# Performance work log

Hardware: AMD Instinct MI355X
Metric: run time of the kernel (lower is better)

## Reference

```python
import jax, jax.numpy as jnp
import numpy as np

D_MODEL = 512
N_HEAD = 8
D_HEAD = D_MODEL // N_HEAD
EPS = 1e-6


def setup_inputs() -> dict:
    key = jax.random.key(0)
    ks = jax.random.split(key, 11)
    b, s, d = 4, 8192, D_MODEL
    scale = 1.0 / np.sqrt(d)
    inp = {
        "q": jax.random.normal(ks[0], (b, s, d), jnp.float32),
        "k": jax.random.normal(ks[1], (b, s, d), jnp.float32),
        "v": jax.random.normal(ks[2], (b, s, d), jnp.float32),
        "Wq": jax.random.normal(ks[3], (d, d), jnp.float32) * scale,
        "bq": jax.random.normal(ks[4], (d,), jnp.float32) * 0.01,
        "Wk": jax.random.normal(ks[5], (d, d), jnp.float32) * scale,
        "bk": jax.random.normal(ks[6], (d,), jnp.float32) * 0.01,
        "Wv": jax.random.normal(ks[7], (d, d), jnp.float32) * scale,
        "bv": jax.random.normal(ks[8], (d,), jnp.float32) * 0.01,
        "Wo": jax.random.normal(ks[9], (d, d), jnp.float32) * scale,
        "bo": jax.random.normal(ks[10], (d,), jnp.float32) * 0.01,
    }
    return inp


def reference(q, k, v, Wq, bq, Wk, bk, Wv, bv, Wo, bo):
    b, s, d = q.shape
    # torch nn.Linear: x @ W.T + b
    feat = lambda x, W, bias: jax.nn.elu(
        (x @ W.T + bias).reshape(b, s, N_HEAD, D_HEAD)) + 1.0
    queries = feat(q, Wq, bq)                      # [b,s,h,dh]
    keys = feat(k, Wk, bk)                         # [b,s,h,dh]
    values = (v @ Wv.T + bv).reshape(b, s, N_HEAD, D_HEAD)
    # full-sequence KV summary state
    k_v = jnp.einsum('bshd,bshm->bhdm', keys, values)   # [b,h,dh,dh]
    z = keys.sum(axis=1, keepdims=True)                 # [b,1,h,dh]
    num = jnp.einsum('bshd,bhdm->bshm', queries, k_v)   # [b,s,h,dh]
    den = jnp.sum(queries * z, axis=-1)                 # [b,s,h] (broadcast over s)
    out = num / (den[..., None] + EPS)
    out = out.reshape(b, s, d)
    return (out @ Wo.T + bo, k_v, z)
```

## Files before the change

kernel.cpp:

```cpp
#include <hip/hip_runtime.h>
#include <hip/hip_bf16.h>
#include <stdint.h>

typedef __bf16 bf16x8 __attribute__((ext_vector_type(8)));
typedef float f32x4 __attribute__((ext_vector_type(4)));

#define S_LEN 8192
#define BATCH 4
#define DMODEL 512
#define NHEAD 8
#define DHEAD 64
#define MROWS (BATCH * S_LEN)
#define OUT0_ELEMS (MROWS * DMODEL)
#define KV_ELEMS (BATCH * NHEAD * DHEAD * DHEAD)
#define Z_ELEMS (BATCH * NHEAD * DHEAD)

__device__ __forceinline__ uint16_t f2bf(float f) {
    uint32_t u = __float_as_uint(f);
    u = (u + 0x7fffu + ((u >> 16) & 1u)) >> 16;
    return (uint16_t)u;
}
__device__ __forceinline__ uint32_t pack2(float a, float b) {
    union { __hip_bfloat162 h; uint32_t u; } cv;
    cv.h = __float22bfloat162_rn(make_float2(a, b));
    return cv.u;
}
__device__ __forceinline__ void gload_lds16(const void* g, void* l) {
    __builtin_amdgcn_global_load_lds(
        (const __attribute__((address_space(1))) void*)g,
        (__attribute__((address_space(3))) void*)l, 16, 0, 0);
}

__global__ void wconv_kernel(const float* __restrict__ w0, const float* __restrict__ w1,
                             const float* __restrict__ w2, const float* __restrict__ w3,
                             uint16_t* __restrict__ dst) {
    const float* src = (blockIdx.y == 0) ? w0 : (blockIdx.y == 1) ? w1
                       : (blockIdx.y == 2) ? w2 : w3;
    uint16_t* d = dst + (size_t)blockIdx.y * (DMODEL * DMODEL);
    int i = (blockIdx.x * 256 + threadIdx.x) * 4;
    float4 v = *(const float4*)(src + i);
    uint2 o;
    o.x = pack2(v.x, v.y);
    o.y = pack2(v.z, v.w);
    *(uint2*)(d + i) = o;
}

template<bool A_F32, bool ELU1, bool OUT_F32, bool OUT_TRANS>
__global__ __launch_bounds__(256, 3)
void gemm_kernel(const void* __restrict__ Ap, const uint16_t* __restrict__ Wb,
                 const float* __restrict__ bias, void* __restrict__ Cp)
{
    __shared__ uint4 smem4[1280];
    uint16_t* sA = (uint16_t*)smem4;
    uint16_t* sB = (uint16_t*)(smem4 + 512);
    const int tid = threadIdx.x;
    const int lane = tid & 63, w = tid >> 6;
    const int quad = lane >> 4, l15 = lane & 15;
    const int m_blk = blockIdx.x * 128, n_blk = blockIdx.y * 128;

    f32x4 acc[4][4];
#pragma unroll
    for (int mi = 0; mi < 4; ++mi)
#pragma unroll
        for (int ni = 0; ni < 4; ++ni) acc[mi][ni] = (f32x4){0.f, 0.f, 0.f, 0.f};

    const int ar = tid >> 1;
    const int ah = tid & 1;
    const int g0 = w * 2;

    const float* arow_base = A_F32 ? ((const float*)Ap + (size_t)(m_blk + ar) * 512 + ah * 16)
                                   : nullptr;
    float4 a0, a1, a2, a3;
    if (A_F32) {
        a0 = *(const float4*)(arow_base);
        a1 = *(const float4*)(arow_base + 4);
        a2 = *(const float4*)(arow_base + 8);
        a3 = *(const float4*)(arow_base + 12);
    }

    for (int kk = 0; kk < 16; ++kk) {
        const int k0 = kk * 32;
        uint4 p0, p1;
        float4 b0, b1, b2, b3;
        if (A_F32) {
            if (kk < 15) {
                const float* arow = arow_base + (kk + 1) * 32;
                b0 = *(const float4*)(arow);
                b1 = *(const float4*)(arow + 4);
                b2 = *(const float4*)(arow + 8);
                b3 = *(const float4*)(arow + 12);
            }
            p0 = make_uint4(pack2(a0.x, a0.y), pack2(a0.z, a0.w),
                            pack2(a1.x, a1.y), pack2(a1.z, a1.w));
            p1 = make_uint4(pack2(a2.x, a2.y), pack2(a2.z, a2.w),
                            pack2(a3.x, a3.y), pack2(a3.z, a3.w));
        }
        __syncthreads();
        gload_lds16(Wb + (size_t)(n_blk + g0 * 16 + l15) * 512 + k0 + quad * 8,
                    sB + g0 * 512);
        gload_lds16(Wb + (size_t)(n_blk + (g0 + 1) * 16 + l15) * 512 + k0 + quad * 8,
                    sB + (g0 + 1) * 512);
        if (A_F32) {
            uint16_t* base = sA + (((ar >> 4) * 4 + ah * 2) * 16 + (ar & 15)) * 8;
            *(uint4*)base = p0;
            *(uint4*)(base + 128) = p1;
            if (kk < 15) { a0 = b0; a1 = b1; a2 = b2; a3 = b3; }
        } else {
            const uint16_t* Ab = (const uint16_t*)Ap;
            gload_lds16(Ab + (size_t)(m_blk + g0 * 16 + l15) * 512 + k0 + quad * 8,
                        sA + g0 * 512);
            gload_lds16(Ab + (size_t)(m_blk + (g0 + 1) * 16 + l15) * 512 + k0 + quad * 8,
                        sA + (g0 + 1) * 512);
        }
        __syncthreads();
        bf16x8 afr[4], bfr[4];
#pragma unroll
        for (int mi = 0; mi < 4; ++mi)
            afr[mi] = *(const bf16x8*)(sA + (((w & 1) * 4 + mi) * 64 + lane) * 8);
#pragma unroll
        for (int ni = 0; ni < 4; ++ni)
            bfr[ni] = *(const bf16x8*)(sB + (((w >> 1) * 4 + ni) * 64 + lane) * 8);
#pragma unroll
        for (int mi = 0; mi < 4; ++mi)
#pragma unroll
            for (int ni = 0; ni < 4; ++ni)
                acc[mi][ni] = __builtin_amdgcn_mfma_f32_16x16x32_bf16(
                    afr[mi], bfr[ni], acc[mi][ni], 0, 0, 0);
    }
    __syncthreads();

    const int mw = (w & 1) * 64, nw = (w >> 1) * 64;
    float bias4[4];
#pragma unroll
    for (int ni = 0; ni < 4; ++ni) bias4[ni] = bias[n_blk + nw + ni * 16 + l15];

    if (OUT_TRANS) {
        uint16_t* t = (uint16_t*)smem4 + w * 2560;
        uint16_t* C = (uint16_t*)Cp;
        const int bb = m_blk >> 13;
        const int s_base = (m_blk & 8191) + mw;
#pragma unroll
        for (int p = 0; p < 2; ++p) {
#pragma unroll
            for (int mi2 = 0; mi2 < 2; ++mi2) {
                const int mi = p * 2 + mi2;
#pragma unroll
                for (int ni = 0; ni < 4; ++ni)
#pragma unroll
                    for (int r = 0; r < 4; ++r) {
                        float val = acc[mi][ni][r] + bias4[ni];
                        if (ELU1) val = (val > 0.f) ? (val + 1.f) : __expf(val);
                        t[(ni * 16 + l15) * 40 + mi2 * 16 + quad * 4 + r] = f2bf(val);
                    }
            }
#pragma unroll
            for (int it = 0; it < 4; ++it) {
                const int idx = it * 64 + lane;
                const int col = idx >> 2, sg = idx & 3;
                uint4 vv = *(const uint4*)(t + col * 40 + sg * 8);
                *(uint4*)(C + ((size_t)(bb * 512) + n_blk + nw + col) * 8192
                            + s_base + p * 32 + sg * 8) = vv;
            }
        }
    } else if (OUT_F32) {
        float* t = (float*)(smem4 + w * 256);
        float* C = (float*)Cp;
#pragma unroll
        for (int mi = 0; mi < 4; ++mi) {
#pragma unroll
            for (int ni = 0; ni < 4; ++ni)
#pragma unroll
                for (int r = 0; r < 4; ++r) {
                    float val = acc[mi][ni][r] + bias4[ni];
                    if (ELU1) val = (val > 0.f) ? (val + 1.f) : __expf(val);
                    t[(quad * 4 + r) * 64 + ni * 16 + l15] = val;
                }
#pragma unroll
            for (int c = 0; c < 4; ++c) {
                const int idx = c * 64 + lane;
                const int row = idx >> 4, colc = (idx & 15) * 4;
                float4 vv = *(const float4*)(t + row * 64 + colc);
                *(float4*)(C + (size_t)(m_blk + mw + mi * 16 + row) * 512
                             + n_blk + nw + colc) = vv;
            }
        }
    } else {
        uint16_t* t = (uint16_t*)(smem4 + w * 128);
        uint16_t* C = (uint16_t*)Cp;
#pragma unroll
        for (int mi = 0; mi < 4; ++mi) {
#pragma unroll
            for (int ni = 0; ni < 4; ++ni)
#pragma unroll
                for (int r = 0; r < 4; ++r) {
                    float val = acc[mi][ni][r] + bias4[ni];
                    if (ELU1) val = (val > 0.f) ? (val + 1.f) : __expf(val);
                    t[(quad * 4 + r) * 64 + ni * 16 + l15] = f2bf(val);
                }
#pragma unroll
            for (int c = 0; c < 2; ++c) {
                const int idx = c * 64 + lane;
                const int row = idx >> 3, colc = (idx & 7) * 8;
                uint4 vv = *(const uint4*)(t + row * 64 + colc);
                *(uint4*)(C + (size_t)(m_blk + mw + mi * 16 + row) * 512
                            + n_blk + nw + colc) = vv;
            }
        }
    }
}

__global__ __launch_bounds__(256)
void kv_kernel(const uint16_t* __restrict__ KT, const uint16_t* __restrict__ VT,
               float* __restrict__ kvz)
{
    __shared__ uint16_t sA[4096];
    __shared__ uint16_t sB[4096];
    const int tid = threadIdx.x;
    const int lane = tid & 63, w = tid >> 6;
    const int quad = lane >> 4, l15 = lane & 15;
    const int bh = blockIdx.y, b = bh >> 3, h = bh & 7;
    const int dh2 = w & 1, mh2 = w >> 1;
    const int S0 = blockIdx.x * 512;

    const uint16_t* Arow = KT + ((size_t)(b * 512 + h * 64 + w * 16 + l15)) * 8192 + S0;
    const uint16_t* Brow = VT + ((size_t)(b * 512 + h * 64 + w * 16 + l15)) * 8192 + S0;

    f32x4 acc[2][2], accz[2];
#pragma unroll
    for (int mi = 0; mi < 2; ++mi) {
        accz[mi] = (f32x4){0.f, 0.f, 0.f, 0.f};
#pragma unroll
        for (int ni = 0; ni < 2; ++ni) acc[mi][ni] = (f32x4){0.f, 0.f, 0.f, 0.f};
    }
    bf16x8 ones;
#pragma unroll
    for (int j = 0; j < 8; ++j) ones[j] = (__bf16)1.0f;

    for (int it = 0; it < 8; ++it) {
        const int soff = it * 64;
        __syncthreads();
#pragma unroll
        for (int c = 0; c < 2; ++c) {
            gload_lds16(Arow + soff + (quad + 4 * c) * 8, sA + (w * 2 + c) * 512);
            gload_lds16(Brow + soff + (quad + 4 * c) * 8, sB + (w * 2 + c) * 512);
        }
        __syncthreads();
#pragma unroll
        for (int kk = 0; kk < 2; ++kk) {
            bf16x8 afr[2], bfr[2];
#pragma unroll
            for (int mi = 0; mi < 2; ++mi)
                afr[mi] = *(const bf16x8*)(sA + (((dh2 * 2 + mi) * 2 + kk) * 64 + lane) * 8);
#pragma unroll
            for (int ni = 0; ni < 2; ++ni)
                bfr[ni] = *(const bf16x8*)(sB + (((mh2 * 2 + ni) * 2 + kk) * 64 + lane) * 8);
#pragma unroll
            for (int mi = 0; mi < 2; ++mi)
#pragma unroll
                for (int ni = 0; ni < 2; ++ni)
                    acc[mi][ni] = __builtin_amdgcn_mfma_f32_16x16x32_bf16(
                        afr[mi], bfr[ni], acc[mi][ni], 0, 0, 0);
            if (mh2 == 0) {
#pragma unroll
                for (int mi = 0; mi < 2; ++mi)
                    accz[mi] = __builtin_amdgcn_mfma_f32_16x16x32_bf16(
                        afr[mi], ones, accz[mi], 0, 0, 0);
            }
        }
    }
    float* kvp = kvz + (size_t)bh * 4096;
#pragma unroll
    for (int mi = 0; mi < 2; ++mi)
#pragma unroll
        for (int ni = 0; ni < 2; ++ni)
#pragma unroll
            for (int r = 0; r < 4; ++r)
                atomicAdd(kvp + (dh2 * 32 + mi * 16 + quad * 4 + r) * 64
                              + mh2 * 32 + ni * 16 + l15, acc[mi][ni][r]);
    if (mh2 == 0 && l15 == 0) {
#pragma unroll
        for (int mi = 0; mi < 2; ++mi)
#pragma unroll
            for (int r = 0; r < 4; ++r)
                atomicAdd(kvz + KV_ELEMS + bh * 64 + dh2 * 32 + mi * 16 + quad * 4 + r,
                          accz[mi][r]);
    }
}

__global__ void kvf_kernel(const float* __restrict__ kvz, uint16_t* __restrict__ KVf) {
    const int bh = blockIdx.x;
    const int tid = threadIdx.x;
    for (int e = tid; e < 5120; e += 256) {
        const int j = e & 7, c = e >> 3;
        const int l15c = c & 15, quadc = (c >> 4) & 3, kkc = (c >> 6) & 1, ng = c >> 7;
        const int n = ng * 16 + l15c;
        const int d = kkc * 32 + quadc * 8 + j;
        float val = (n < 64) ? kvz[(size_t)bh * 4096 + d * 64 + n]
                  : ((n == 64) ? kvz[KV_ELEMS + bh * 64 + d] : 0.f);
        KVf[(size_t)bh * 5120 + e] = f2bf(val);
    }
}

__global__ __launch_bounds__(256, 4)
void attn_kernel(const uint16_t* __restrict__ Qb, const uint16_t* __restrict__ KVf,
                 uint16_t* __restrict__ Yb)
{
    __shared__ uint4 smem4[1152];
    uint16_t* sB = (uint16_t*)smem4;
    uint16_t* sEp = (uint16_t*)(smem4 + 640);
    const int bh = blockIdx.y;
    const int b = bh >> 3, h = bh & 7;
    const int tid = threadIdx.x;
    const int lane = tid & 63, w = tid >> 6, quad = lane >> 4, l15 = lane & 15;

    const uint16_t* src = KVf + (size_t)bh * 5120;
    gload_lds16(src + (size_t)tid * 8,         sB + (w * 64) * 8);
    gload_lds16(src + (size_t)(256 + tid) * 8, sB + ((256 + w * 64)) * 8);
    if (tid < 128)
        gload_lds16(src + (size_t)(512 + tid) * 8, sB + ((512 + w * 64)) * 8);
    __syncthreads();

    f32x4 acc[2][5];
#pragma unroll
    for (int mi = 0; mi < 2; ++mi)
#pragma unroll
        for (int ni = 0; ni < 5; ++ni) acc[mi][ni] = (f32x4){0.f, 0.f, 0.f, 0.f};
    const int row0 = blockIdx.x * 128 + w * 32;
#pragma unroll
    for (int kk = 0; kk < 2; ++kk) {
        bf16x8 afr[2];
#pragma unroll
        for (int mi = 0; mi < 2; ++mi) {
            const size_t ga = (size_t)(b * S_LEN + row0 + mi * 16 + l15) * DMODEL
                              + h * DHEAD + kk * 32 + quad * 8;
            afr[mi] = *(const bf16x8*)(Qb + ga);
        }
#pragma unroll
        for (int ni = 0; ni < 5; ++ni) {
            bf16x8 bfr = *(const bf16x8*)(sB + ((ni * 2 + kk) * 64 + lane) * 8);
            acc[0][ni] = __builtin_amdgcn_mfma_f32_16x16x32_bf16(afr[0], bfr, acc[0][ni], 0, 0, 0);
            acc[1][ni] = __builtin_amdgcn_mfma_f32_16x16x32_bf16(afr[1], bfr, acc[1][ni], 0, 0, 0);
        }
    }
    uint16_t* t = sEp + w * 1024;
#pragma unroll
    for (int mi = 0; mi < 2; ++mi) {
        float rden[4];
#pragma unroll
        for (int r = 0; r < 4; ++r) {
            const float den = __shfl(acc[mi][4][r], lane & 48, 64);
            rden[r] = 1.0f / (den + 1e-6f);
        }
#pragma unroll
        for (int ni = 0; ni < 4; ++ni)
#pragma unroll
            for (int r = 0; r < 4; ++r)
                t[(quad * 4 + r) * 64 + ni * 16 + l15] = f2bf(acc[mi][ni][r] * rden[r]);
#pragma unroll
        for (int c = 0; c < 2; ++c) {
            const int idx = c * 64 + lane;
            const int row = idx >> 3, colc = (idx & 7) * 8;
            uint4 vv = *(const uint4*)(t + row * 64 + colc);
            *(uint4*)(Yb + (size_t)(b * S_LEN + row0 + mi * 16 + row) * 512
                        + h * DHEAD + colc) = vv;
        }
    }
}

extern "C" void kernel_launch(void* const* d_in, const int* in_sizes, int n_in,
                              void* d_out, int out_size, void* d_ws, size_t ws_size,
                              hipStream_t stream)
{
    const float* q  = (const float*)d_in[0];
    const float* k  = (const float*)d_in[1];
    const float* v  = (const float*)d_in[2];
    const float* Wq = (const float*)d_in[3];
    const float* bq = (const float*)d_in[4];
    const float* Wk = (const float*)d_in[5];
    const float* bk = (const float*)d_in[6];
    const float* Wv = (const float*)d_in[7];
    const float* bv = (const float*)d_in[8];
    const float* Wo = (const float*)d_in[9];
    const float* bo = (const float*)d_in[10];

    uint16_t* Qb = (uint16_t*)d_ws;
    uint16_t* KT = Qb + OUT0_ELEMS;
    uint16_t* VT = KT + OUT0_ELEMS;
    uint16_t* Wb = VT + OUT0_ELEMS;
    uint16_t* KVf = VT;
    uint16_t* Yb = KT;

    float* out0 = (float*)d_out;
    float* kvz  = out0 + OUT0_ELEMS;

    hipMemsetAsync(kvz, 0, (KV_ELEMS + Z_ELEMS) * sizeof(float), stream);
    wconv_kernel<<<dim3(256, 4), 256, 0, stream>>>(Wq, Wk, Wv, Wo, Wb);
    gemm_kernel<true, true,  false, false><<<dim3(256, 4), 256, 0, stream>>>(q, Wb,              bq, Qb);
    gemm_kernel<true, true,  false, true ><<<dim3(256, 4), 256, 0, stream>>>(k, Wb + 262144,     bk, KT);
    gemm_kernel<true, false, false, true ><<<dim3(256, 4), 256, 0, stream>>>(v, Wb + 2 * 262144, bv, VT);
    kv_kernel<<<dim3(16, 32), 256, 0, stream>>>(KT, VT, kvz);
    kvf_kernel<<<dim3(32), 256, 0, stream>>>(kvz, KVf);
    attn_kernel<<<dim3(64, 32), 256, 0, stream>>>(Qb, KVf, Yb);
    gemm_kernel<false, false, true, false><<<dim3(256, 4), 256, 0, stream>>>(Yb, Wb + 3 * 262144, bo, out0);
}
```

Baseline: 416.2 us.

## Load A fragments directly to registers and stage full weight K-slab in LDS

The GEMM kernel stops staging the activation tile in shared memory. Each wave loads its A fragments straight from global memory into registers with one-step prefetch, and the whole 128x512 weight slab is staged in LDS in two halves, so the k-loop needs two barriers instead of thirty-two. The KV reduction kernel likewise drops LDS and reads K/V fragments directly into registers with prefetch, removing its per-iteration barriers. In exchange, LDS use grows to 64KB per block (occupancy hint lowered to 2), and each activation element is now fetched from global memory twice, once by each of the two waves sharing those rows.

```diff
diff --git a/kernel.cpp b/kernel.cpp
--- a/kernel.cpp
+++ b/kernel.cpp
@@ -46,17 +46,17 @@
 }
 
 template<bool A_F32, bool ELU1, bool OUT_F32, bool OUT_TRANS>
-__global__ __launch_bounds__(256, 3)
+__global__ __launch_bounds__(256, 2)
 void gemm_kernel(const void* __restrict__ Ap, const uint16_t* __restrict__ Wb,
                  const float* __restrict__ bias, void* __restrict__ Cp)
 {
-    __shared__ uint4 smem4[1280];
-    uint16_t* sA = (uint16_t*)smem4;
-    uint16_t* sB = (uint16_t*)(smem4 + 512);
+    __shared__ uint4 smem4[4096];
+    uint16_t* sB = (uint16_t*)smem4;
     const int tid = threadIdx.x;
     const int lane = tid & 63, w = tid >> 6;
     const int quad = lane >> 4, l15 = lane & 15;
     const int m_blk = blockIdx.x * 128, n_blk = blockIdx.y * 128;
+    const int mw = (w & 1) * 64, nw = (w >> 1) * 64;
 
     f32x4 acc[4][4];
 #pragma unroll
@@ -64,72 +64,85 @@
 #pragma unroll
         for (int ni = 0; ni < 4; ++ni) acc[mi][ni] = (f32x4){0.f, 0.f, 0.f, 0.f};
 
-    const int ar = tid >> 1;
-    const int ah = tid & 1;
-    const int g0 = w * 2;
-
-    const float* arow_base = A_F32 ? ((const float*)Ap + (size_t)(m_blk + ar) * 512 + ah * 16)
-                                   : nullptr;
-    float4 a0, a1, a2, a3;
-    if (A_F32) {
-        a0 = *(const float4*)(arow_base);
-        a1 = *(const float4*)(arow_base + 4);
-        a2 = *(const float4*)(arow_base + 8);
-        a3 = *(const float4*)(arow_base + 12);
-    }
-
-    for (int kk = 0; kk < 16; ++kk) {
-        const int k0 = kk * 32;
-        uint4 p0, p1;
-        float4 b0, b1, b2, b3;
+    const float* a32[4];
+    const uint16_t* a16[4];
+#pragma unroll
+    for (int mi = 0; mi < 4; ++mi) {
+        const size_t row = (size_t)(m_blk + mw + mi * 16 + l15);
+        if (A_F32) a32[mi] = (const float*)Ap + row * 512 + quad * 8;
+        else       a16[mi] = (const uint16_t*)Ap + row * 512 + quad * 8;
+    }
+
+    float4 ac[4][2];
+    uint4  ac16[4];
+#pragma unroll
+    for (int mi = 0; mi < 4; ++mi) {
         if (A_F32) {
-            if (kk < 15) {
-                const float* arow = arow_base + (kk + 1) * 32;
-                b0 = *(const float4*)(arow);
-                b1 = *(const float4*)(arow + 4);
-                b2 = *(const float4*)(arow + 8);
-                b3 = *(const float4*)(arow + 12);
-            }
-            p0 = make_uint4(pack2(a0.x, a0.y), pack2(a0.z, a0.w),
-                            pack2(a1.x, a1.y), pack2(a1.z, a1.w));
-            p1 = make_uint4(pack2(a2.x, a2.y), pack2(a2.z, a2.w),
-                            pack2(a3.x, a3.y), pack2(a3.z, a3.w));
+            ac[mi][0] = *(const float4*)(a32[mi]);
+            ac[mi][1] = *(const float4*)(a32[mi] + 4);
+        } else {
+            ac16[mi] = *(const uint4*)(a16[mi]);
+        }
+    }
+
+#pragma unroll
+    for (int h = 0; h < 2; ++h) {
+        if (h) __syncthreads();
+#pragma unroll
+        for (int t = 0; t < 16; ++t) {
+            const int f = w * 16 + t;
+            const int nl = f >> 3, kkl = f & 7;
+            gload_lds16(Wb + (size_t)(n_blk + nl * 16 + l15) * 512 + h * 256 + kkl * 32 + quad * 8,
+                        sB + f * 512);
         }
         __syncthreads();
-        gload_lds16(Wb + (size_t)(n_blk + g0 * 16 + l15) * 512 + k0 + quad * 8,
-                    sB + g0 * 512);
-        gload_lds16(Wb + (size_t)(n_blk + (g0 + 1) * 16 + l15) * 512 + k0 + quad * 8,
-                    sB + (g0 + 1) * 512);
-        if (A_F32) {
-            uint16_t* base = sA + (((ar >> 4) * 4 + ah * 2) * 16 + (ar & 15)) * 8;
-            *(uint4*)base = p0;
-            *(uint4*)(base + 128) = p1;
-            if (kk < 15) { a0 = b0; a1 = b1; a2 = b2; a3 = b3; }
-        } else {
-            const uint16_t* Ab = (const uint16_t*)Ap;
-            gload_lds16(Ab + (size_t)(m_blk + g0 * 16 + l15) * 512 + k0 + quad * 8,
-                        sA + g0 * 512);
-            gload_lds16(Ab + (size_t)(m_blk + (g0 + 1) * 16 + l15) * 512 + k0 + quad * 8,
-                        sA + (g0 + 1) * 512);
-        }
-        __syncthreads();
-        bf16x8 afr[4], bfr[4];
-#pragma unroll
-        for (int mi = 0; mi < 4; ++mi)
-            afr[mi] = *(const bf16x8*)(sA + (((w & 1) * 4 + mi) * 64 + lane) * 8);
-#pragma unroll
-        for (int ni = 0; ni < 4; ++ni)
-            bfr[ni] = *(const bf16x8*)(sB + (((w >> 1) * 4 + ni) * 64 + lane) * 8);
-#pragma unroll
-        for (int mi = 0; mi < 4; ++mi)
-#pragma unroll
-            for (int ni = 0; ni < 4; ++ni)
-                acc[mi][ni] = __builtin_amdgcn_mfma_f32_16x16x32_bf16(
-                    afr[mi], bfr[ni], acc[mi][ni], 0, 0, 0);
+#pragma unroll
+        for (int kkl = 0; kkl < 8; ++kkl) {
+            const int kkg = h * 8 + kkl;
+            float4 an[4][2];
+            uint4  an16[4];
+            if (kkg < 15) {
+#pragma unroll
+                for (int mi = 0; mi < 4; ++mi) {
+                    if (A_F32) {
+                        an[mi][0] = *(const float4*)(a32[mi] + (kkg + 1) * 32);
+                        an[mi][1] = *(const float4*)(a32[mi] + (kkg + 1) * 32 + 4);
+                    } else {
+                        an16[mi] = *(const uint4*)(a16[mi] + (kkg + 1) * 32);
+                    }
+                }
+            }
+            bf16x8 afr[4];
+#pragma unroll
+            for (int mi = 0; mi < 4; ++mi) {
+                union { uint4 u; bf16x8 v; } cv;
+                if (A_F32) {
+                    cv.u = make_uint4(pack2(ac[mi][0].x, ac[mi][0].y), pack2(ac[mi][0].z, ac[mi][0].w),
+                                      pack2(ac[mi][1].x, ac[mi][1].y), pack2(ac[mi][1].z, ac[mi][1].w));
+                } else {
+                    cv.u = ac16[mi];
+                }
+                afr[mi] = cv.v;
+            }
+#pragma unroll
+            for (int ni = 0; ni < 4; ++ni) {
+                const bf16x8 bfr = *(const bf16x8*)(sB + ((((w >> 1) * 4 + ni) * 8 + kkl) * 64 + lane) * 8);
+#pragma unroll
+                for (int mi = 0; mi < 4; ++mi)
+                    acc[mi][ni] = __builtin_amdgcn_mfma_f32_16x16x32_bf16(
+                        afr[mi], bfr, acc[mi][ni], 0, 0, 0);
+            }
+            if (kkg < 15) {
+#pragma unroll
+                for (int mi = 0; mi < 4; ++mi) {
+                    if (A_F32) { ac[mi][0] = an[mi][0]; ac[mi][1] = an[mi][1]; }
+                    else       { ac16[mi] = an16[mi]; }
+                }
+            }
+        }
     }
     __syncthreads();
 
-    const int mw = (w & 1) * 64, nw = (w >> 1) * 64;
     float bias4[4];
 #pragma unroll
     for (int ni = 0; ni < 4; ++ni) bias4[ni] = bias[n_blk + nw + ni * 16 + l15];
@@ -209,12 +222,10 @@
     }
 }
 
-__global__ __launch_bounds__(256)
+__global__ __launch_bounds__(256, 4)
 void kv_kernel(const uint16_t* __restrict__ KT, const uint16_t* __restrict__ VT,
                float* __restrict__ kvz)
 {
-    __shared__ uint16_t sA[4096];
-    __shared__ uint16_t sB[4096];
     const int tid = threadIdx.x;
     const int lane = tid & 63, w = tid >> 6;
     const int quad = lane >> 4, l15 = lane & 15;
@@ -222,8 +233,13 @@
     const int dh2 = w & 1, mh2 = w >> 1;
     const int S0 = blockIdx.x * 512;
 
-    const uint16_t* Arow = KT + ((size_t)(b * 512 + h * 64 + w * 16 + l15)) * 8192 + S0;
-    const uint16_t* Brow = VT + ((size_t)(b * 512 + h * 64 + w * 16 + l15)) * 8192 + S0;
+    const uint16_t* Ka[2];
+    const uint16_t* Va[2];
+#pragma unroll
+    for (int i = 0; i < 2; ++i) {
+        Ka[i] = KT + (size_t)(b * 512 + h * 64 + dh2 * 32 + i * 16 + l15) * 8192 + S0 + quad * 8;
+        Va[i] = VT + (size_t)(b * 512 + h * 64 + mh2 * 32 + i * 16 + l15) * 8192 + S0 + quad * 8;
+    }
 
     f32x4 acc[2][2], accz[2];
 #pragma unroll
@@ -236,36 +252,45 @@
 #pragma unroll
     for (int j = 0; j < 8; ++j) ones[j] = (__bf16)1.0f;
 
-    for (int it = 0; it < 8; ++it) {
-        const int soff = it * 64;
-        __syncthreads();
-#pragma unroll
-        for (int c = 0; c < 2; ++c) {
-            gload_lds16(Arow + soff + (quad + 4 * c) * 8, sA + (w * 2 + c) * 512);
-            gload_lds16(Brow + soff + (quad + 4 * c) * 8, sB + (w * 2 + c) * 512);
-        }
-        __syncthreads();
-#pragma unroll
-        for (int kk = 0; kk < 2; ++kk) {
-            bf16x8 afr[2], bfr[2];
+    uint4 ka[2], va[2];
+#pragma unroll
+    for (int i = 0; i < 2; ++i) {
+        ka[i] = *(const uint4*)(Ka[i]);
+        va[i] = *(const uint4*)(Va[i]);
+    }
+
+#pragma unroll
+    for (int it = 0; it < 16; ++it) {
+        uint4 kn[2], vn[2];
+        if (it < 15) {
+#pragma unroll
+            for (int i = 0; i < 2; ++i) {
+                kn[i] = *(const uint4*)(Ka[i] + (it + 1) * 32);
+                vn[i] = *(const uint4*)(Va[i] + (it + 1) * 32);
+            }
+        }
+        bf16x8 afr[2], bfr[2];
+#pragma unroll
+        for (int i = 0; i < 2; ++i) {
+            union { uint4 u; bf16x8 v; } ca, cb;
+            ca.u = ka[i]; afr[i] = ca.v;
+            cb.u = va[i]; bfr[i] = cb.v;
+        }
+#pragma unroll
+        for (int mi = 0; mi < 2; ++mi)
+#pragma unroll
+            for (int ni = 0; ni < 2; ++ni)
+                acc[mi][ni] = __builtin_amdgcn_mfma_f32_16x16x32_bf16(
+                    afr[mi], bfr[ni], acc[mi][ni], 0, 0, 0);
+        if (mh2 == 0) {
 #pragma unroll
             for (int mi = 0; mi < 2; ++mi)
-                afr[mi] = *(const bf16x8*)(sA + (((dh2 * 2 + mi) * 2 + kk) * 64 + lane) * 8);
-#pragma unroll
-            for (int ni = 0; ni < 2; ++ni)
-                bfr[ni] = *(const bf16x8*)(sB + (((mh2 * 2 + ni) * 2 + kk) * 64 + lane) * 8);
-#pragma unroll
-            for (int mi = 0; mi < 2; ++mi)
-#pragma unroll
-                for (int ni = 0; ni < 2; ++ni)
-                    acc[mi][ni] = __builtin_amdgcn_mfma_f32_16x16x32_bf16(
-                        afr[mi], bfr[ni], acc[mi][ni], 0, 0, 0);
-            if (mh2 == 0) {
-#pragma unroll
-                for (int mi = 0; mi < 2; ++mi)
-                    accz[mi] = __builtin_amdgcn_mfma_f32_16x16x32_bf16(
-                        afr[mi], ones, accz[mi], 0, 0, 0);
-            }
+                accz[mi] = __builtin_amdgcn_mfma_f32_16x16x32_bf16(
+                    afr[mi], ones, accz[mi], 0, 0, 0);
+        }
+        if (it < 15) {
+#pragma unroll
+            for (int i = 0; i < 2; ++i) { ka[i] = kn[i]; va[i] = vn[i]; }
         }
     }
     float* kvp = kvz + (size_t)bh * 4096;
```

Result: slower. 501.1 us (+20.4%).

## Double-buffer GEMM LDS tiles and load KV fragments directly into registers

Applied to the files above, without the earlier changes.

The projection GEMM moves from single-buffered LDS staging with two barriers per k-step to a ping-pong pair of A/B LDS buffers. The next tile's loads and packs now overlap the MFMA work on the current tile, with one barrier per half-step. The kv_kernel drops LDS entirely: each wave reads its K/V fragments straight from global memory into registers with one-step prefetch, and it gains a launch-bounds occupancy hint. The costs are more LDS per GEMM block, which can lower occupancy, and redundant global reads in kv_kernel because waves no longer share staged tiles.

```diff
diff --git a/kernel.cpp b/kernel.cpp
--- a/kernel.cpp
+++ b/kernel.cpp
@@ -50,13 +50,16 @@
 void gemm_kernel(const void* __restrict__ Ap, const uint16_t* __restrict__ Wb,
                  const float* __restrict__ bias, void* __restrict__ Cp)
 {
-    __shared__ uint4 smem4[1280];
-    uint16_t* sA = (uint16_t*)smem4;
-    uint16_t* sB = (uint16_t*)(smem4 + 512);
+    __shared__ uint4 smem4[2048];
+    uint16_t* sA0 = (uint16_t*)smem4;
+    uint16_t* sB0 = sA0 + 4096;
+    uint16_t* sA1 = sB0 + 4096;
+    uint16_t* sB1 = sA1 + 4096;
     const int tid = threadIdx.x;
     const int lane = tid & 63, w = tid >> 6;
     const int quad = lane >> 4, l15 = lane & 15;
     const int m_blk = blockIdx.x * 128, n_blk = blockIdx.y * 128;
+    const int g0 = w * 2;
 
     f32x4 acc[4][4];
 #pragma unroll
@@ -66,53 +69,39 @@
 
     const int ar = tid >> 1;
     const int ah = tid & 1;
-    const int g0 = w * 2;
-
     const float* arow_base = A_F32 ? ((const float*)Ap + (size_t)(m_blk + ar) * 512 + ah * 16)
                                    : nullptr;
-    float4 a0, a1, a2, a3;
-    if (A_F32) {
-        a0 = *(const float4*)(arow_base);
-        a1 = *(const float4*)(arow_base + 4);
-        a2 = *(const float4*)(arow_base + 8);
-        a3 = *(const float4*)(arow_base + 12);
-    }
-
-    for (int kk = 0; kk < 16; ++kk) {
-        const int k0 = kk * 32;
-        uint4 p0, p1;
-        float4 b0, b1, b2, b3;
-        if (A_F32) {
-            if (kk < 15) {
-                const float* arow = arow_base + (kk + 1) * 32;
-                b0 = *(const float4*)(arow);
-                b1 = *(const float4*)(arow + 4);
-                b2 = *(const float4*)(arow + 8);
-                b3 = *(const float4*)(arow + 12);
-            }
-            p0 = make_uint4(pack2(a0.x, a0.y), pack2(a0.z, a0.w),
-                            pack2(a1.x, a1.y), pack2(a1.z, a1.w));
-            p1 = make_uint4(pack2(a2.x, a2.y), pack2(a2.z, a2.w),
-                            pack2(a3.x, a3.y), pack2(a3.z, a3.w));
-        }
-        __syncthreads();
+    const uint16_t* Ab = (const uint16_t*)Ap;
+
+    auto loadA = [&](int t, float4* r) {
+        const float* p = arow_base + t * 32;
+        r[0] = *(const float4*)(p);
+        r[1] = *(const float4*)(p + 4);
+        r[2] = *(const float4*)(p + 8);
+        r[3] = *(const float4*)(p + 12);
+    };
+    auto packA = [&](uint16_t* sA, const float4* r) {
+        uint16_t* base = sA + (((ar >> 4) * 4 + ah * 2) * 16 + (ar & 15)) * 8;
+        *(uint4*)base = make_uint4(pack2(r[0].x, r[0].y), pack2(r[0].z, r[0].w),
+                                   pack2(r[1].x, r[1].y), pack2(r[1].z, r[1].w));
+        *(uint4*)(base + 128) = make_uint4(pack2(r[2].x, r[2].y), pack2(r[2].z, r[2].w),
+                                           pack2(r[3].x, r[3].y), pack2(r[3].z, r[3].w));
+    };
+    auto stageB = [&](uint16_t* sB, int t) {
+        const int k0 = t * 32;
         gload_lds16(Wb + (size_t)(n_blk + g0 * 16 + l15) * 512 + k0 + quad * 8,
                     sB + g0 * 512);
         gload_lds16(Wb + (size_t)(n_blk + (g0 + 1) * 16 + l15) * 512 + k0 + quad * 8,
                     sB + (g0 + 1) * 512);
-        if (A_F32) {
-            uint16_t* base = sA + (((ar >> 4) * 4 + ah * 2) * 16 + (ar & 15)) * 8;
-            *(uint4*)base = p0;
-            *(uint4*)(base + 128) = p1;
-            if (kk < 15) { a0 = b0; a1 = b1; a2 = b2; a3 = b3; }
-        } else {
-            const uint16_t* Ab = (const uint16_t*)Ap;
-            gload_lds16(Ab + (size_t)(m_blk + g0 * 16 + l15) * 512 + k0 + quad * 8,
-                        sA + g0 * 512);
-            gload_lds16(Ab + (size_t)(m_blk + (g0 + 1) * 16 + l15) * 512 + k0 + quad * 8,
-                        sA + (g0 + 1) * 512);
-        }
-        __syncthreads();
+    };
+    auto stageA16 = [&](uint16_t* sA, int t) {
+        const int k0 = t * 32;
+        gload_lds16(Ab + (size_t)(m_blk + g0 * 16 + l15) * 512 + k0 + quad * 8,
+                    sA + g0 * 512);
+        gload_lds16(Ab + (size_t)(m_blk + (g0 + 1) * 16 + l15) * 512 + k0 + quad * 8,
+                    sA + (g0 + 1) * 512);
+    };
+    auto compute = [&](const uint16_t* sA, const uint16_t* sB) {
         bf16x8 afr[4], bfr[4];
 #pragma unroll
         for (int mi = 0; mi < 4; ++mi)
@@ -126,8 +115,32 @@
             for (int ni = 0; ni < 4; ++ni)
                 acc[mi][ni] = __builtin_amdgcn_mfma_f32_16x16x32_bf16(
                     afr[mi], bfr[ni], acc[mi][ni], 0, 0, 0);
-    }
+    };
+
+    float4 rX[4], rY[4];
+    if (A_F32) loadA(0, rY);
+    stageB(sB0, 0);
+    if (A_F32) { loadA(1, rX); packA(sA0, rY); }
+    else       stageA16(sA0, 0);
     __syncthreads();
+
+    for (int p = 0; p < 8; ++p) {
+        const int t0 = 2 * p;
+        if (A_F32 && p < 7) loadA(t0 + 2, rY);
+        stageB(sB1, t0 + 1);
+        if (A_F32) packA(sA1, rX);
+        else       stageA16(sA1, t0 + 1);
+        compute(sA0, sB0);
+        __syncthreads();
+        if (p < 7) {
+            if (A_F32) loadA(t0 + 3, rX);
+            stageB(sB0, t0 + 2);
+            if (A_F32) packA(sA0, rY);
+            else       stageA16(sA0, t0 + 2);
+        }
+        compute(sA1, sB1);
+        __syncthreads();
+    }
 
     const int mw = (w & 1) * 64, nw = (w >> 1) * 64;
     float bias4[4];
@@ -209,12 +222,10 @@
     }
 }
 
-__global__ __launch_bounds__(256)
+__global__ __launch_bounds__(256, 4)
 void kv_kernel(const uint16_t* __restrict__ KT, const uint16_t* __restrict__ VT,
                float* __restrict__ kvz)
 {
-    __shared__ uint16_t sA[4096];
-    __shared__ uint16_t sB[4096];
     const int tid = threadIdx.x;
     const int lane = tid & 63, w = tid >> 6;
     const int quad = lane >> 4, l15 = lane & 15;
@@ -222,8 +233,13 @@
     const int dh2 = w & 1, mh2 = w >> 1;
     const int S0 = blockIdx.x * 512;
 
-    const uint16_t* Arow = KT + ((size_t)(b * 512 + h * 64 + w * 16 + l15)) * 8192 + S0;
-    const uint16_t* Brow = VT + ((size_t)(b * 512 + h * 64 + w * 16 + l15)) * 8192 + S0;
+    const uint16_t* Ka[2];
+    const uint16_t* Va[2];
+#pragma unroll
+    for (int i = 0; i < 2; ++i) {
+        Ka[i] = KT + (size_t)(b * 512 + h * 64 + dh2 * 32 + i * 16 + l15) * 8192 + S0 + quad * 8;
+        Va[i] = VT + (size_t)(b * 512 + h * 64 + mh2 * 32 + i * 16 + l15) * 8192 + S0 + quad * 8;
+    }
 
     f32x4 acc[2][2], accz[2];
 #pragma unroll
@@ -236,36 +252,45 @@
 #pragma unroll
     for (int j = 0; j < 8; ++j) ones[j] = (__bf16)1.0f;
 
-    for (int it = 0; it < 8; ++it) {
-        const int soff = it * 64;
-        __syncthreads();
-#pragma unroll
-        for (int c = 0; c < 2; ++c) {
-            gload_lds16(Arow + soff + (quad + 4 * c) * 8, sA + (w * 2 + c) * 512);
-            gload_lds16(Brow + soff + (quad + 4 * c) * 8, sB + (w * 2 + c) * 512);
-        }
-        __syncthreads();
-#pragma unroll
-        for (int kk = 0; kk < 2; ++kk) {
-            bf16x8 afr[2], bfr[2];
+    uint4 ka[2], va[2];
+#pragma unroll
+    for (int i = 0; i < 2; ++i) {
+        ka[i] = *(const uint4*)(Ka[i]);
+        va[i] = *(const uint4*)(Va[i]);
+    }
+
+#pragma unroll
+    for (int it = 0; it < 16; ++it) {
+        uint4 kn[2], vn[2];
+        if (it < 15) {
+#pragma unroll
+            for (int i = 0; i < 2; ++i) {
+                kn[i] = *(const uint4*)(Ka[i] + (it + 1) * 32);
+                vn[i] = *(const uint4*)(Va[i] + (it + 1) * 32);
+            }
+        }
+        bf16x8 afr[2], bfr[2];
+#pragma unroll
+        for (int i = 0; i < 2; ++i) {
+            union { uint4 u; bf16x8 v; } ca, cb;
+            ca.u = ka[i]; afr[i] = ca.v;
+            cb.u = va[i]; bfr[i] = cb.v;
+        }
+#pragma unroll
+        for (int mi = 0; mi < 2; ++mi)
+#pragma unroll
+            for (int ni = 0; ni < 2; ++ni)
+                acc[mi][ni] = __builtin_amdgcn_mfma_f32_16x16x32_bf16(
+                    afr[mi], bfr[ni], acc[mi][ni], 0, 0, 0);
+        if (mh2 == 0) {
 #pragma unroll
             for (int mi = 0; mi < 2; ++mi)
-                afr[mi] = *(const bf16x8*)(sA + (((dh2 * 2 + mi) * 2 + kk) * 64 + lane) * 8);
-#pragma unroll
-            for (int ni = 0; ni < 2; ++ni)
-                bfr[ni] = *(const bf16x8*)(sB + (((mh2 * 2 + ni) * 2 + kk) * 64 + lane) * 8);
-#pragma unroll
-            for (int mi = 0; mi < 2; ++mi)
-#pragma unroll
-                for (int ni = 0; ni < 2; ++ni)
-                    acc[mi][ni] = __builtin_amdgcn_mfma_f32_16x16x32_bf16(
-                        afr[mi], bfr[ni], acc[mi][ni], 0, 0, 0);
-            if (mh2 == 0) {
-#pragma unroll
-                for (int mi = 0; mi < 2; ++mi)
-                    accz[mi] = __builtin_amdgcn_mfma_f32_16x16x32_bf16(
-                        afr[mi], ones, accz[mi], 0, 0, 0);
-            }
+                accz[mi] = __builtin_amdgcn_mfma_f32_16x16x32_bf16(
+                    afr[mi], ones, accz[mi], 0, 0, 0);
+        }
+        if (it < 15) {
+#pragma unroll
+            for (int i = 0; i < 2; ++i) { ka[i] = kn[i]; va[i] = vn[i]; }
         }
     }
     float* kvp = kvz + (size_t)bh * 4096;
```

Measured after the change: 430.6 us. 3.5% more time.
